# Performance work log

Hardware: AMD Instinct MI355X
Metric: run time of the kernel (lower is better)

## Reference

```python
import jax, jax.numpy as jnp
import numpy as np


def conv2d(x, w, b, pad):
    # NCHW / OIHW conv, stride 1
    y = jax.lax.conv_general_dilated(x, w, (1, 1), [(pad, pad), (pad, pad)],
                                     dimension_numbers=('NCHW', 'OIHW', 'NCHW'))
    return y + b[None, :, None, None]


def deform_conv2d(x, offset, modulator, w_reg, b_reg):
    # Faithful reimplementation of torchvision.ops.deform_conv2d (stride=1,
    # pad=K//2, dilation=1, 1 offset group), offset layout [B, 2*K*K, H, W]
    # with (dy, dx) pairs per kernel tap.
    B, C, H, W = x.shape
    K = w_reg.shape[-1]
    KK = K * K
    pad = K // 2
    off = offset.reshape(B, KK, 2, H, W)
    ks_y = (jnp.arange(KK) // K - pad).astype(x.dtype)
    ks_x = (jnp.arange(KK) % K - pad).astype(x.dtype)
    hh = jnp.arange(H, dtype=x.dtype)
    ww = jnp.arange(W, dtype=x.dtype)
    # sampling coords per (batch, kernel tap, out_y, out_x)
    py = hh[None, None, :, None] + ks_y[None, :, None, None] + off[:, :, 0]
    px = ww[None, None, None, :] + ks_x[None, :, None, None] + off[:, :, 1]
    y0 = jnp.floor(py)
    x0 = jnp.floor(px)
    ly = py - y0
    lx = px - x0
    y0i = y0.astype(jnp.int32)
    x0i = x0.astype(jnp.int32)
    x_flat = x.reshape(B, C, H * W)

    def gather(yi, xi, wgt):
        valid = (yi >= 0) & (yi < H) & (xi >= 0) & (xi < W)
        idx = (jnp.clip(yi, 0, H - 1) * W + jnp.clip(xi, 0, W - 1)).reshape(B, KK, H * W)
        v = jnp.take_along_axis(x_flat[:, :, None, :], idx[:, None], axis=3)  # [B,C,KK,HW]
        w = (wgt * valid.astype(x.dtype)).reshape(B, 1, KK, H * W)
        return v * w

    v = (gather(y0i, x0i, (1 - ly) * (1 - lx))
         + gather(y0i, x0i + 1, (1 - ly) * lx)
         + gather(y0i + 1, x0i, ly * (1 - lx))
         + gather(y0i + 1, x0i + 1, ly * lx))
    v = v * modulator.reshape(B, 1, KK, H * W)
    out = jnp.einsum('bckn,ock->bon', v, w_reg.reshape(w_reg.shape[0], C, KK))
    return out.reshape(B, -1, H, W) + b_reg[None, :, None, None]


def setup_inputs() -> dict:
    key = jax.random.key(0)
    ks = jax.random.split(key, 14)
    B, C, H, W = 8, 256, 64, 64
    K = 3
    Cr = C // 4  # SE ratio=4
    x = jax.random.normal(ks[0], (B, C, H, W), jnp.float32)
    # small offset-conv weights keep sampled offsets modest (torchvision inits these to 0)
    w_off = jax.random.normal(ks[1], (2 * K * K, C, K, K), jnp.float32) * 0.01
    b_off = jax.random.normal(ks[2], (2 * K * K,), jnp.float32) * 0.01
    w_mod = jax.random.normal(ks[3], (K * K, C, K, K), jnp.float32) * 0.01
    b_mod = jax.random.normal(ks[4], (K * K,), jnp.float32) * 0.01
    w_reg = jax.random.normal(ks[5], (C, C, K, K), jnp.float32) * (1.0 / np.sqrt(C * K * K))
    b_reg = jax.random.normal(ks[6], (C,), jnp.float32) * 0.01
    w_se1 = jax.random.normal(ks[7], (Cr, C), jnp.float32) * (1.0 / np.sqrt(C))
    b_se1 = jnp.zeros((Cr,), jnp.float32)
    w_se2 = jax.random.normal(ks[8], (C, Cr), jnp.float32) * (1.0 / np.sqrt(Cr))
    b_se2 = jnp.zeros((C,), jnp.float32)
    w_mask = jax.random.normal(ks[9], (C, C, 1, 1), jnp.float32) * (1.0 / np.sqrt(C))
    b_mask = jnp.zeros((C,), jnp.float32)
    return {"x": x, "w_off": w_off, "b_off": b_off, "w_mod": w_mod, "b_mod": b_mod,
            "w_reg": w_reg, "b_reg": b_reg, "w_se1": w_se1, "b_se1": b_se1,
            "w_se2": w_se2, "b_se2": b_se2, "w_mask": w_mask, "b_mask": b_mask}


def reference(x, w_off, b_off, w_mod, b_mod, w_reg, b_reg,
              w_se1, b_se1, w_se2, b_se2, w_mask, b_mask):
    # DeformableConv2d
    offset = conv2d(x, w_off, b_off, pad=1)
    modulator = 2.0 * jax.nn.sigmoid(conv2d(x, w_mod, b_mod, pad=1))
    f = deform_conv2d(x, offset, modulator, w_reg, b_reg)
    # SEBlock('avg', ch, ratio=4)
    s = jnp.mean(f, axis=(2, 3))                       # [B, C]
    s = jax.nn.relu(s @ w_se1.T + b_se1)               # [B, C/4]
    s = jax.nn.sigmoid(s @ w_se2.T + b_se2)            # [B, C]
    f = f * s[:, :, None, None]
    # mask = Hardsigmoid(Conv1x1(x))
    m = conv2d(x, w_mask, b_mask, pad=0)
    m = jnp.clip(m / 6.0 + 0.5, 0.0, 1.0)
    return f * m + x
```

## Files before the change

kernel.cpp:

```cpp
#include <hip/hip_runtime.h>
#include <math.h>

#define HWSZ 4096
#define C_ 256
#define B_ 8

#define M_WS      0
#define XB_WS     4194304
#define WT2_WS    8388608
#define SMEAN_WS  8753152
#define SSCALE_WS 8755200

typedef __attribute__((ext_vector_type(8))) short short8;
typedef __attribute__((ext_vector_type(4))) float f32x4;

__device__ __forceinline__ uint bfr(float a) {
  uint u = __float_as_uint(a);
  return (u + 0x7fffu + ((u >> 16) & 1u)) >> 16;
}
__device__ __forceinline__ uint pk2(float a, float b) { return bfr(a) | (bfr(b) << 16); }
__device__ __forceinline__ float bff(ushort u) { return __uint_as_float((uint)u << 16); }
__device__ __forceinline__ float lo16(uint u) { return __uint_as_float(u << 16); }
__device__ __forceinline__ float hi16(uint u) { return __uint_as_float(u & 0xffff0000u); }

__global__ __launch_bounds__(256) void k0_weights(
    const float* __restrict__ w_reg, const float* __restrict__ w_mask,
    const float* __restrict__ w_off, const float* __restrict__ w_mod,
    float* __restrict__ ws) {
  int i = blockIdx.x * 256 + threadIdx.x;
  const int nwt = 10 * 65536;
  const int total = nwt + 9 * 32 * 256;
  if (i >= total) {
    int z = i - total;
    if (z < 2048) ws[SMEAN_WS + z] = 0.f;
    return;
  }
  float v;
  if (i < 9 * 65536) {
    int kk = i >> 16, o = (i >> 8) & 255, c = i & 255;
    v = w_reg[(o * C_ + c) * 9 + kk];
  } else if (i < nwt) {
    v = w_mask[i - 9 * 65536];
  } else {
    int e = i - nwt;
    int s = e >> 13, r = e & 8191;
    int o2 = r >> 8, c = r & 255;
    if (o2 < 18)      v = w_off[(o2 * C_ + c) * 9 + s];
    else if (o2 < 27) v = w_mod[((o2 - 18) * C_ + c) * 9 + s];
    else              v = 0.f;
  }
  ((ushort*)(ws + WT2_WS))[i] = (ushort)bfr(v);
}

__global__ __launch_bounds__(256) void k0b_nhwc(const float* __restrict__ x,
                                                float* __restrict__ ws) {
  __shared__ float tile[64][65];
  int b = blockIdx.x >> 6, hw0 = (blockIdx.x & 63) << 6;
  int t = threadIdx.x;
  uint* xb = (uint*)(ws + XB_WS) + ((size_t)b << 19);
  int rr = t >> 6, cc = t & 63;
  int e = t & 7, hwp = t >> 3;
  for (int cg = 0; cg < 4; cg++) {
    __syncthreads();
    const float* xp = x + ((size_t)(b * 256 + cg * 64 + rr)) * HWSZ + hw0 + cc;
    #pragma unroll
    for (int r0 = 0; r0 < 64; r0 += 4)
      tile[r0 + rr][cc] = xp[(size_t)r0 * HWSZ];
    __syncthreads();
    #pragma unroll
    for (int h2 = 0; h2 < 2; h2++) {
      int hw_l = h2 * 32 + hwp;
      int c2 = e * 8;
      uint4 val;
      val.x = pk2(tile[c2][hw_l], tile[c2 + 1][hw_l]);
      val.y = pk2(tile[c2 + 2][hw_l], tile[c2 + 3][hw_l]);
      val.z = pk2(tile[c2 + 4][hw_l], tile[c2 + 5][hw_l]);
      val.w = pk2(tile[c2 + 6][hw_l], tile[c2 + 7][hw_l]);
      *(uint4*)&xb[(size_t)(hw0 + hw_l) * 128 + cg * 32 + e * 4] = val;
    }
  }
}

__global__ __launch_bounds__(512, 4) void k2_fused(
    const float* __restrict__ b_off, const float* __restrict__ b_mod,
    const float* __restrict__ b_reg, const float* __restrict__ b_mask,
    float* __restrict__ ws, float* __restrict__ out) {
  __shared__ uint  vbuf32[64 * 128];
  __shared__ float offmod[27 * 64];
  __shared__ int   midx[9 * 4 * 64];
  __shared__ float mwgt[9 * 4 * 64];

  int bl = ((blockIdx.x & 7) << 6) | (blockIdx.x >> 3);
  int b = bl >> 6, h = bl & 63;
  int t = threadIdx.x;
  int lane = t & 63, w = t >> 6;
  const int hwid = (w << 1) | (lane >> 5);
  const int cl = lane & 31;
  const ushort* xb2 = (const ushort*)(ws + XB_WS) + ((size_t)b << 20);
  const ushort* wt2 = (const ushort*)(ws + WT2_WS);
  const ushort* wom = wt2 + 10 * 65536;
  const int fr = lane & 15, fq = lane >> 4;

  f32x4 aom = (f32x4)0.f;
  const int m0 = w >> 2, nt0 = w & 3;
  for (int s = 0; s < 9; s++) {
    int row = h + s / 3 - 1;
    uint4 pv[4];
    #pragma unroll
    for (int p = 0; p < 4; p++) {
      int n = p * 16 + hwid;
      int col = n + s % 3 - 1;
      uint4 d = make_uint4(0, 0, 0, 0);
      if (((unsigned)row < 64u) && ((unsigned)col < 64u))
        d = *(const uint4*)(xb2 + ((size_t)(row * 64 + col)) * 256 + cl * 8);
      pv[p] = d;
    }
    __syncthreads();
    #pragma unroll
    for (int p = 0; p < 4; p++) {
      int n = p * 16 + hwid;
      vbuf32[n * 128 + (((uint)(cl * 4)) ^ ((uint)(n & 7) << 2)) + 0] = pv[p].x;
      *(uint4*)&vbuf32[n * 128 + (((uint)(cl * 4)) ^ ((uint)(n & 7) << 2))] = pv[p];
    }
    __syncthreads();
    const ushort* wp = wom + (size_t)s * 8192;
    for (int ks = 0; ks < 8; ks++) {
      short8 af = *(const short8*)(wp + (m0 * 16 + fr) * 256 + ks * 32 + fq * 8);
      int bn = nt0 * 16 + fr;
      uint idx = (uint)bn * 128u + (((uint)(ks * 16 + fq * 4)) ^ ((uint)(bn & 7) << 2));
      short8 bf = *(const short8*)&vbuf32[idx];
      aom = __builtin_amdgcn_mfma_f32_16x16x32_bf16(af, bf, aom, 0, 0, 0);
    }
  }
  __syncthreads();
  #pragma unroll
  for (int r = 0; r < 4; r++) {
    int o = m0 * 16 + fq * 4 + r;
    int nn = nt0 * 16 + fr;
    if (o < 18) {
      offmod[o * 64 + nn] = aom[r] + b_off[o];
    } else if (o < 27) {
      float v = aom[r] + b_mod[o - 18];
      offmod[o * 64 + nn] = 2.f / (1.f + expf(-v));
    }
  }
  __syncthreads();

  for (int e = t; e < 576; e += 512) {
    int kk = e >> 6, p = e & 63;
    float dy = offmod[(2 * kk) * 64 + p];
    float dx = offmod[(2 * kk + 1) * 64 + p];
    float md = offmod[(18 + kk) * 64 + p];
    float py = (float)(h + kk / 3 - 1) + dy;
    float px = (float)(p + kk % 3 - 1) + dx;
    float fy = floorf(py), fx = floorf(px);
    float ly = py - fy, lx = px - fx;
    int y0 = (int)fy, x0 = (int)fx;
    int y1 = y0 + 1, x1 = x0 + 1;
    float vy0 = ((unsigned)y0 < 64u) ? 1.f : 0.f;
    float vy1 = ((unsigned)y1 < 64u) ? 1.f : 0.f;
    float vx0 = ((unsigned)x0 < 64u) ? 1.f : 0.f;
    float vx1 = ((unsigned)x1 < 64u) ? 1.f : 0.f;
    int cy0 = min(max(y0, 0), 63), cy1 = min(max(y1, 0), 63);
    int cx0 = min(max(x0, 0), 63), cx1 = min(max(x1, 0), 63);
    int base = kk * 256 + p;
    midx[base]       = cy0 * 64 + cx0;
    midx[base + 64]  = cy0 * 64 + cx1;
    midx[base + 128] = cy1 * 64 + cx0;
    midx[base + 192] = cy1 * 64 + cx1;
    mwgt[base]       = (1.f - ly) * (1.f - lx) * md * vy0 * vx0;
    mwgt[base + 64]  = (1.f - ly) * lx * md * vy0 * vx1;
    mwgt[base + 128] = ly * (1.f - lx) * md * vy1 * vx0;
    mwgt[base + 192] = ly * lx * md * vy1 * vx1;
  }
  __syncthreads();

  f32x4 acc[2][4];
  #pragma unroll
  for (int mt = 0; mt < 2; mt++)
    #pragma unroll
    for (int nt = 0; nt < 4; nt++) acc[mt][nt] = (f32x4)0.f;
  const int o0 = w << 5;

  for (int kk = 0; kk < 9; kk++) {
    uint4 pv[4];
    #pragma unroll
    for (int p = 0; p < 4; p++) {
      int n = p * 16 + hwid;
      int base = kk * 256 + n;
      float a0 = 0.f, a1 = 0.f, a2 = 0.f, a3 = 0.f, a4 = 0.f, a5 = 0.f, a6 = 0.f, a7 = 0.f;
      #pragma unroll
      for (int cr = 0; cr < 4; cr++) {
        int gi = midx[base + cr * 64];
        float wv = mwgt[base + cr * 64];
        uint4 d = *(const uint4*)(xb2 + (size_t)gi * 256 + cl * 8);
        a0 = fmaf(wv, lo16(d.x), a0); a1 = fmaf(wv, hi16(d.x), a1);
        a2 = fmaf(wv, lo16(d.y), a2); a3 = fmaf(wv, hi16(d.y), a3);
        a4 = fmaf(wv, lo16(d.z), a4); a5 = fmaf(wv, hi16(d.z), a5);
        a6 = fmaf(wv, lo16(d.w), a6); a7 = fmaf(wv, hi16(d.w), a7);
      }
      pv[p] = make_uint4(pk2(a0, a1), pk2(a2, a3), pk2(a4, a5), pk2(a6, a7));
    }
    __syncthreads();
    #pragma unroll
    for (int p = 0; p < 4; p++) {
      int n = p * 16 + hwid;
      *(uint4*)&vbuf32[n * 128 + (((uint)(cl * 4)) ^ ((uint)(n & 7) << 2))] = pv[p];
    }
    __syncthreads();
    const ushort* wtap = wt2 + (size_t)kk * 65536;
    for (int ks = 0; ks < 8; ks++) {
      short8 af0 = *(const short8*)(wtap + (o0 + fr) * 256 + ks * 32 + fq * 8);
      short8 af1 = *(const short8*)(wtap + (o0 + 16 + fr) * 256 + ks * 32 + fq * 8);
      #pragma unroll
      for (int nt = 0; nt < 4; nt++) {
        int bn = nt * 16 + fr;
        uint idx = (uint)bn * 128u + (((uint)(ks * 16 + fq * 4)) ^ ((uint)(bn & 7) << 2));
        short8 bf = *(const short8*)&vbuf32[idx];
        acc[0][nt] = __builtin_amdgcn_mfma_f32_16x16x32_bf16(af0, bf, acc[0][nt], 0, 0, 0);
        acc[1][nt] = __builtin_amdgcn_mfma_f32_16x16x32_bf16(af1, bf, acc[1][nt], 0, 0, 0);
      }
    }
  }
  float* sme = ws + SMEAN_WS + b * 256;
  #pragma unroll
  for (int mt = 0; mt < 2; mt++)
    #pragma unroll
    for (int r = 0; r < 4; r++) {
      int o = o0 + mt * 16 + fq * 4 + r;
      float bo = b_reg[o];
      float* op = out + (size_t)(b * C_ + o) * HWSZ + h * 64;
      float so = 0.f;
      #pragma unroll
      for (int nt = 0; nt < 4; nt++) {
        float fv = acc[mt][nt][r] + bo;
        op[nt * 16 + fr] = fv;
        so += fv;
        acc[mt][nt][r] = 0.f;
      }
      so += __shfl_xor(so, 1);
      so += __shfl_xor(so, 2);
      so += __shfl_xor(so, 4);
      so += __shfl_xor(so, 8);
      if (fr == 0) atomicAdd(&sme[o], so);
    }

  {
    uint4 pv[4];
    #pragma unroll
    for (int p = 0; p < 4; p++) {
      int n = p * 16 + hwid;
      pv[p] = *(const uint4*)(xb2 + ((size_t)(h * 64 + n)) * 256 + cl * 8);
    }
    __syncthreads();
    #pragma unroll
    for (int p = 0; p < 4; p++) {
      int n = p * 16 + hwid;
      *(uint4*)&vbuf32[n * 128 + (((uint)(cl * 4)) ^ ((uint)(n & 7) << 2))] = pv[p];
    }
    __syncthreads();
  }
  {
    const ushort* wtap = wt2 + (size_t)9 * 65536;
    for (int ks = 0; ks < 8; ks++) {
      short8 af0 = *(const short8*)(wtap + (o0 + fr) * 256 + ks * 32 + fq * 8);
      short8 af1 = *(const short8*)(wtap + (o0 + 16 + fr) * 256 + ks * 32 + fq * 8);
      #pragma unroll
      for (int nt = 0; nt < 4; nt++) {
        int bn = nt * 16 + fr;
        uint idx = (uint)bn * 128u + (((uint)(ks * 16 + fq * 4)) ^ ((uint)(bn & 7) << 2));
        short8 bf = *(const short8*)&vbuf32[idx];
        acc[0][nt] = __builtin_amdgcn_mfma_f32_16x16x32_bf16(af0, bf, acc[0][nt], 0, 0, 0);
        acc[1][nt] = __builtin_amdgcn_mfma_f32_16x16x32_bf16(af1, bf, acc[1][nt], 0, 0, 0);
      }
    }
  }
  ushort* mws = (ushort*)(ws + M_WS);
  #pragma unroll
  for (int mt = 0; mt < 2; mt++)
    #pragma unroll
    for (int r = 0; r < 4; r++) {
      int o = o0 + mt * 16 + fq * 4 + r;
      float bm = b_mask[o];
      ushort* mp = mws + (size_t)(b * C_ + o) * HWSZ + h * 64;
      #pragma unroll
      for (int nt = 0; nt < 4; nt++) {
        float mv = fminf(fmaxf((acc[mt][nt][r] + bm) * (1.f / 6.f) + 0.5f, 0.f), 1.f);
        mp[nt * 16 + fr] = (ushort)bfr(mv);
      }
    }
}

__global__ __launch_bounds__(256) void k4_se(
    const float* __restrict__ w_se1, const float* __restrict__ b_se1,
    const float* __restrict__ w_se2, const float* __restrict__ b_se2,
    float* __restrict__ ws) {
  __shared__ float sm[2048];
  __shared__ float s1[512];
  int t = threadIdx.x;
  for (int e = t; e < 2048; e += 256) sm[e] = ws[SMEAN_WS + e] * (1.f / HWSZ);
  __syncthreads();
  for (int e = t; e < 512; e += 256) {
    int b = e >> 6, cr = e & 63;
    float a = b_se1[cr];
    for (int c = 0; c < 256; c++) a += sm[b * 256 + c] * w_se1[cr * 256 + c];
    s1[e] = fmaxf(a, 0.f);
  }
  __syncthreads();
  for (int e = t; e < 2048; e += 256) {
    int b = e >> 8, c = e & 255;
    float a = b_se2[c];
    for (int cr = 0; cr < 64; cr++) a += s1[b * 64 + cr] * w_se2[c * 64 + cr];
    ws[SSCALE_WS + e] = 1.f / (1.f + expf(-a));
  }
}

__global__ __launch_bounds__(256) void k5_final(const float* __restrict__ x,
                                                const float* __restrict__ ws,
                                                float* __restrict__ out) {
  const ushort* mws = (const ushort*)(ws + M_WS);
  int i4 = blockIdx.x * 256 + threadIdx.x;
  const int total = B_ * C_ * HWSZ / 4;
  for (; i4 < total; i4 += gridDim.x * 256) {
    int i = i4 * 4;
    int bc = i >> 12;
    float s = ws[SSCALE_WS + bc];
    float4 f = *(const float4*)&out[i];
    uint2 mu = *(const uint2*)&mws[i];
    float4 xv = *(const float4*)&x[i];
    float4 r;
    r.x = f.x * s * bff((ushort)(mu.x & 0xffffu)) + xv.x;
    r.y = f.y * s * bff((ushort)(mu.x >> 16)) + xv.y;
    r.z = f.z * s * bff((ushort)(mu.y & 0xffffu)) + xv.z;
    r.w = f.w * s * bff((ushort)(mu.y >> 16)) + xv.w;
    *(float4*)&out[i] = r;
  }
}

extern "C" void kernel_launch(void* const* d_in, const int* in_sizes, int n_in,
                              void* d_out, int out_size, void* d_ws, size_t ws_size,
                              hipStream_t stream) {
  const float* x      = (const float*)d_in[0];
  const float* w_off  = (const float*)d_in[1];
  const float* b_off  = (const float*)d_in[2];
  const float* w_mod  = (const float*)d_in[3];
  const float* b_mod  = (const float*)d_in[4];
  const float* w_reg  = (const float*)d_in[5];
  const float* b_reg  = (const float*)d_in[6];
  const float* w_se1  = (const float*)d_in[7];
  const float* b_se1  = (const float*)d_in[8];
  const float* w_se2  = (const float*)d_in[9];
  const float* b_se2  = (const float*)d_in[10];
  const float* w_mask = (const float*)d_in[11];
  const float* b_mask = (const float*)d_in[12];
  float* out = (float*)d_out;
  float* ws  = (float*)d_ws;

  k0_weights<<<dim3(2856), dim3(256), 0, stream>>>(w_reg, w_mask, w_off, w_mod, ws);
  k0b_nhwc<<<dim3(512), dim3(256), 0, stream>>>(x, ws);
  k2_fused<<<dim3(512), dim3(512), 0, stream>>>(b_off, b_mod, b_reg, b_mask, ws, out);
  k4_se<<<dim3(1), dim3(256), 0, stream>>>(w_se1, b_se1, w_se2, b_se2, ws);
  k5_final<<<dim3(2048), dim3(256), 0, stream>>>(x, ws, out);
}
```

Baseline: 207.3 us.

## Double-buffer LDS and overlap bilinear gathers with MFMA in fused deform kernel

Replaces the single LDS staging buffer with two ping-pong buffers. Global loads for the next tap (shifted rows for the offset conv, bilinear gathers for the deform conv, centre rows for the mask conv) are issued before the current tap's MFMAs and written to the other buffer afterwards, which cuts the syncs per step from two to one. Sampling indices and weights are now computed per thread in registers instead of being staged in shared-memory tables. The cost is more live registers (eight uint4 gather results plus weights), which could cause spills at launch_bounds(512,4), and the layout doubles the LDS buffer size.

```diff
diff --git a/kernel.cpp b/kernel.cpp
--- a/kernel.cpp
+++ b/kernel.cpp
@@ -85,10 +85,8 @@
     const float* __restrict__ b_off, const float* __restrict__ b_mod,
     const float* __restrict__ b_reg, const float* __restrict__ b_mask,
     float* __restrict__ ws, float* __restrict__ out) {
-  __shared__ uint  vbuf32[64 * 128];
+  __shared__ uint vb[2][64 * 128];
   __shared__ float offmod[27 * 64];
-  __shared__ int   midx[9 * 4 * 64];
-  __shared__ float mwgt[9 * 4 * 64];
 
   int bl = ((blockIdx.x & 7) << 6) | (blockIdx.x >> 3);
   int b = bl >> 6, h = bl & 63;
@@ -101,58 +99,31 @@
   const ushort* wom = wt2 + 10 * 65536;
   const int fr = lane & 15, fq = lane >> 4;
 
-  f32x4 aom = (f32x4)0.f;
-  const int m0 = w >> 2, nt0 = w & 3;
-  for (int s = 0; s < 9; s++) {
+  int nrow[4]; uint widx[4];
+  #pragma unroll
+  for (int p = 0; p < 4; p++) {
+    nrow[p] = p * 16 + hwid;
+    widx[p] = (uint)nrow[p] * 128u + (((uint)cl * 4u) ^ ((uint)(nrow[p] & 7) << 2));
+  }
+
+  auto loadShift = [&](int s, uint4* d) {
     int row = h + s / 3 - 1;
-    uint4 pv[4];
     #pragma unroll
     for (int p = 0; p < 4; p++) {
-      int n = p * 16 + hwid;
-      int col = n + s % 3 - 1;
-      uint4 d = make_uint4(0, 0, 0, 0);
+      int col = nrow[p] + s % 3 - 1;
+      uint4 v = make_uint4(0, 0, 0, 0);
       if (((unsigned)row < 64u) && ((unsigned)col < 64u))
-        d = *(const uint4*)(xb2 + ((size_t)(row * 64 + col)) * 256 + cl * 8);
-      pv[p] = d;
-    }
-    __syncthreads();
-    #pragma unroll
-    for (int p = 0; p < 4; p++) {
-      int n = p * 16 + hwid;
-      vbuf32[n * 128 + (((uint)(cl * 4)) ^ ((uint)(n & 7) << 2)) + 0] = pv[p].x;
-      *(uint4*)&vbuf32[n * 128 + (((uint)(cl * 4)) ^ ((uint)(n & 7) << 2))] = pv[p];
-    }
-    __syncthreads();
-    const ushort* wp = wom + (size_t)s * 8192;
-    for (int ks = 0; ks < 8; ks++) {
-      short8 af = *(const short8*)(wp + (m0 * 16 + fr) * 256 + ks * 32 + fq * 8);
-      int bn = nt0 * 16 + fr;
-      uint idx = (uint)bn * 128u + (((uint)(ks * 16 + fq * 4)) ^ ((uint)(bn & 7) << 2));
-      short8 bf = *(const short8*)&vbuf32[idx];
-      aom = __builtin_amdgcn_mfma_f32_16x16x32_bf16(af, bf, aom, 0, 0, 0);
-    }
-  }
-  __syncthreads();
-  #pragma unroll
-  for (int r = 0; r < 4; r++) {
-    int o = m0 * 16 + fq * 4 + r;
-    int nn = nt0 * 16 + fr;
-    if (o < 18) {
-      offmod[o * 64 + nn] = aom[r] + b_off[o];
-    } else if (o < 27) {
-      float v = aom[r] + b_mod[o - 18];
-      offmod[o * 64 + nn] = 2.f / (1.f + expf(-v));
-    }
-  }
-  __syncthreads();
-
-  for (int e = t; e < 576; e += 512) {
-    int kk = e >> 6, p = e & 63;
-    float dy = offmod[(2 * kk) * 64 + p];
-    float dx = offmod[(2 * kk + 1) * 64 + p];
-    float md = offmod[(18 + kk) * 64 + p];
+        v = *(const uint4*)(xb2 + ((size_t)(row * 64 + col)) * 256 + cl * 8);
+      d[p] = v;
+    }
+  };
+  auto makeRecs = [&](int kk, int p, float* wg, int* ix) {
+    int n = nrow[p];
+    float dy = offmod[(2 * kk) * 64 + n];
+    float dx = offmod[(2 * kk + 1) * 64 + n];
+    float md = offmod[(18 + kk) * 64 + n];
     float py = (float)(h + kk / 3 - 1) + dy;
-    float px = (float)(p + kk % 3 - 1) + dx;
+    float px = (float)(n + kk % 3 - 1) + dx;
     float fy = floorf(py), fx = floorf(px);
     float ly = py - fy, lx = px - fx;
     int y0 = (int)fy, x0 = (int)fx;
@@ -163,15 +134,60 @@
     float vx1 = ((unsigned)x1 < 64u) ? 1.f : 0.f;
     int cy0 = min(max(y0, 0), 63), cy1 = min(max(y1, 0), 63);
     int cx0 = min(max(x0, 0), 63), cx1 = min(max(x1, 0), 63);
-    int base = kk * 256 + p;
-    midx[base]       = cy0 * 64 + cx0;
-    midx[base + 64]  = cy0 * 64 + cx1;
-    midx[base + 128] = cy1 * 64 + cx0;
-    midx[base + 192] = cy1 * 64 + cx1;
-    mwgt[base]       = (1.f - ly) * (1.f - lx) * md * vy0 * vx0;
-    mwgt[base + 64]  = (1.f - ly) * lx * md * vy0 * vx1;
-    mwgt[base + 128] = ly * (1.f - lx) * md * vy1 * vx0;
-    mwgt[base + 192] = ly * lx * md * vy1 * vx1;
+    ix[0] = cy0 * 64 + cx0; wg[0] = (1.f - ly) * (1.f - lx) * md * vy0 * vx0;
+    ix[1] = cy0 * 64 + cx1; wg[1] = (1.f - ly) * lx * md * vy0 * vx1;
+    ix[2] = cy1 * 64 + cx0; wg[2] = ly * (1.f - lx) * md * vy1 * vx0;
+    ix[3] = cy1 * 64 + cx1; wg[3] = ly * lx * md * vy1 * vx1;
+  };
+  auto combine = [&](const uint4* d, const float* wg) -> uint4 {
+    float a0 = 0.f, a1 = 0.f, a2 = 0.f, a3 = 0.f, a4 = 0.f, a5 = 0.f, a6 = 0.f, a7 = 0.f;
+    #pragma unroll
+    for (int cr = 0; cr < 4; cr++) {
+      uint4 dd = d[cr]; float wv = wg[cr];
+      a0 = fmaf(wv, lo16(dd.x), a0); a1 = fmaf(wv, hi16(dd.x), a1);
+      a2 = fmaf(wv, lo16(dd.y), a2); a3 = fmaf(wv, hi16(dd.y), a3);
+      a4 = fmaf(wv, lo16(dd.z), a4); a5 = fmaf(wv, hi16(dd.z), a5);
+      a6 = fmaf(wv, lo16(dd.w), a6); a7 = fmaf(wv, hi16(dd.w), a7);
+    }
+    return make_uint4(pk2(a0, a1), pk2(a2, a3), pk2(a4, a5), pk2(a6, a7));
+  };
+
+  f32x4 aom = (f32x4)0.f;
+  const int m0 = w >> 2, nt0 = w & 3;
+  {
+    uint4 sd[4];
+    loadShift(0, sd);
+    #pragma unroll
+    for (int p = 0; p < 4; p++) *(uint4*)&vb[0][widx[p]] = sd[p];
+    __syncthreads();
+    for (int s = 0; s < 9; s++) {
+      if (s < 8) loadShift(s + 1, sd);
+      const uint cur = s & 1;
+      const ushort* wp = wom + (size_t)s * 8192;
+      for (int ks = 0; ks < 8; ks++) {
+        short8 af = *(const short8*)(wp + (m0 * 16 + fr) * 256 + ks * 32 + fq * 8);
+        int bn = nt0 * 16 + fr;
+        uint idx = (uint)bn * 128u + (((uint)(ks * 16 + fq * 4)) ^ ((uint)(bn & 7) << 2));
+        short8 bf = *(const short8*)&vb[cur][idx];
+        aom = __builtin_amdgcn_mfma_f32_16x16x32_bf16(af, bf, aom, 0, 0, 0);
+      }
+      if (s < 8) {
+        #pragma unroll
+        for (int p = 0; p < 4; p++) *(uint4*)&vb[(s & 1) ^ 1][widx[p]] = sd[p];
+      }
+      __syncthreads();
+    }
+  }
+  #pragma unroll
+  for (int r = 0; r < 4; r++) {
+    int o = m0 * 16 + fq * 4 + r;
+    int nn = nt0 * 16 + fr;
+    if (o < 18) {
+      offmod[o * 64 + nn] = aom[r] + b_off[o];
+    } else if (o < 27) {
+      float v = aom[r] + b_mod[o - 18];
+      offmod[o * 64 + nn] = 2.f / (1.f + expf(-v));
+    }
   }
   __syncthreads();
 
@@ -181,101 +197,122 @@
     #pragma unroll
     for (int nt = 0; nt < 4; nt++) acc[mt][nt] = (f32x4)0.f;
   const int o0 = w << 5;
-
-  for (int kk = 0; kk < 9; kk++) {
-    uint4 pv[4];
+  float* sme = ws + SMEAN_WS + b * 256;
+  ushort* mws = (ushort*)(ws + M_WS);
+
+  {
     #pragma unroll
     for (int p = 0; p < 4; p++) {
-      int n = p * 16 + hwid;
-      int base = kk * 256 + n;
-      float a0 = 0.f, a1 = 0.f, a2 = 0.f, a3 = 0.f, a4 = 0.f, a5 = 0.f, a6 = 0.f, a7 = 0.f;
-      #pragma unroll
-      for (int cr = 0; cr < 4; cr++) {
-        int gi = midx[base + cr * 64];
-        float wv = mwgt[base + cr * 64];
-        uint4 d = *(const uint4*)(xb2 + (size_t)gi * 256 + cl * 8);
-        a0 = fmaf(wv, lo16(d.x), a0); a1 = fmaf(wv, hi16(d.x), a1);
-        a2 = fmaf(wv, lo16(d.y), a2); a3 = fmaf(wv, hi16(d.y), a3);
-        a4 = fmaf(wv, lo16(d.z), a4); a5 = fmaf(wv, hi16(d.z), a5);
-        a6 = fmaf(wv, lo16(d.w), a6); a7 = fmaf(wv, hi16(d.w), a7);
-      }
-      pv[p] = make_uint4(pk2(a0, a1), pk2(a2, a3), pk2(a4, a5), pk2(a6, a7));
-    }
-    __syncthreads();
-    #pragma unroll
-    for (int p = 0; p < 4; p++) {
-      int n = p * 16 + hwid;
-      *(uint4*)&vbuf32[n * 128 + (((uint)(cl * 4)) ^ ((uint)(n & 7) << 2))] = pv[p];
-    }
-    __syncthreads();
+      float wg[4]; int ix[4];
+      makeRecs(0, p, wg, ix);
+      uint4 d[4];
+      #pragma unroll
+      for (int cr = 0; cr < 4; cr++)
+        d[cr] = *(const uint4*)(xb2 + (size_t)ix[cr] * 256 + cl * 8);
+      *(uint4*)&vb[0][widx[p]] = combine(d, wg);
+    }
+  }
+  __syncthreads();
+
+  for (int kk = 0; kk < 10; kk++) {
+    const uint cur = kk & 1, nxt = cur ^ 1;
     const ushort* wtap = wt2 + (size_t)kk * 65536;
-    for (int ks = 0; ks < 8; ks++) {
+    const int nk = kk + 1;
+    uint4 d[8];
+    float wg01[8];
+    if (nk < 9) {
+      #pragma unroll
+      for (int p = 0; p < 2; p++) {
+        float wg[4]; int ix[4];
+        makeRecs(nk, p, wg, ix);
+        #pragma unroll
+        for (int cr = 0; cr < 4; cr++) {
+          d[p * 4 + cr] = *(const uint4*)(xb2 + (size_t)ix[cr] * 256 + cl * 8);
+          wg01[p * 4 + cr] = wg[cr];
+        }
+      }
+    } else if (nk == 9) {
+      #pragma unroll
+      for (int p = 0; p < 2; p++)
+        d[p * 4] = *(const uint4*)(xb2 + ((size_t)(h * 64 + nrow[p])) * 256 + cl * 8);
+    }
+    for (int ks = 0; ks < 4; ks++) {
       short8 af0 = *(const short8*)(wtap + (o0 + fr) * 256 + ks * 32 + fq * 8);
       short8 af1 = *(const short8*)(wtap + (o0 + 16 + fr) * 256 + ks * 32 + fq * 8);
       #pragma unroll
       for (int nt = 0; nt < 4; nt++) {
         int bn = nt * 16 + fr;
         uint idx = (uint)bn * 128u + (((uint)(ks * 16 + fq * 4)) ^ ((uint)(bn & 7) << 2));
-        short8 bf = *(const short8*)&vbuf32[idx];
+        short8 bf = *(const short8*)&vb[cur][idx];
         acc[0][nt] = __builtin_amdgcn_mfma_f32_16x16x32_bf16(af0, bf, acc[0][nt], 0, 0, 0);
         acc[1][nt] = __builtin_amdgcn_mfma_f32_16x16x32_bf16(af1, bf, acc[1][nt], 0, 0, 0);
       }
     }
-  }
-  float* sme = ws + SMEAN_WS + b * 256;
-  #pragma unroll
-  for (int mt = 0; mt < 2; mt++)
-    #pragma unroll
-    for (int r = 0; r < 4; r++) {
-      int o = o0 + mt * 16 + fq * 4 + r;
-      float bo = b_reg[o];
-      float* op = out + (size_t)(b * C_ + o) * HWSZ + h * 64;
-      float so = 0.f;
-      #pragma unroll
-      for (int nt = 0; nt < 4; nt++) {
-        float fv = acc[mt][nt][r] + bo;
-        op[nt * 16 + fr] = fv;
-        so += fv;
-        acc[mt][nt][r] = 0.f;
-      }
-      so += __shfl_xor(so, 1);
-      so += __shfl_xor(so, 2);
-      so += __shfl_xor(so, 4);
-      so += __shfl_xor(so, 8);
-      if (fr == 0) atomicAdd(&sme[o], so);
-    }
-
-  {
-    uint4 pv[4];
-    #pragma unroll
-    for (int p = 0; p < 4; p++) {
-      int n = p * 16 + hwid;
-      pv[p] = *(const uint4*)(xb2 + ((size_t)(h * 64 + n)) * 256 + cl * 8);
-    }
-    __syncthreads();
-    #pragma unroll
-    for (int p = 0; p < 4; p++) {
-      int n = p * 16 + hwid;
-      *(uint4*)&vbuf32[n * 128 + (((uint)(cl * 4)) ^ ((uint)(n & 7) << 2))] = pv[p];
-    }
-    __syncthreads();
-  }
-  {
-    const ushort* wtap = wt2 + (size_t)9 * 65536;
-    for (int ks = 0; ks < 8; ks++) {
+    if (nk < 9) {
+      *(uint4*)&vb[nxt][widx[0]] = combine(&d[0], &wg01[0]);
+      *(uint4*)&vb[nxt][widx[1]] = combine(&d[4], &wg01[4]);
+      #pragma unroll
+      for (int p = 2; p < 4; p++) {
+        float wg[4]; int ix[4];
+        makeRecs(nk, p, wg, ix);
+        #pragma unroll
+        for (int cr = 0; cr < 4; cr++) {
+          d[(p - 2) * 4 + cr] = *(const uint4*)(xb2 + (size_t)ix[cr] * 256 + cl * 8);
+          wg01[(p - 2) * 4 + cr] = wg[cr];
+        }
+      }
+    } else if (nk == 9) {
+      *(uint4*)&vb[nxt][widx[0]] = d[0];
+      *(uint4*)&vb[nxt][widx[1]] = d[4];
+      #pragma unroll
+      for (int p = 2; p < 4; p++)
+        d[(p - 2) * 4] = *(const uint4*)(xb2 + ((size_t)(h * 64 + nrow[p])) * 256 + cl * 8);
+    }
+    for (int ks = 4; ks < 8; ks++) {
       short8 af0 = *(const short8*)(wtap + (o0 + fr) * 256 + ks * 32 + fq * 8);
       short8 af1 = *(const short8*)(wtap + (o0 + 16 + fr) * 256 + ks * 32 + fq * 8);
       #pragma unroll
       for (int nt = 0; nt < 4; nt++) {
         int bn = nt * 16 + fr;
         uint idx = (uint)bn * 128u + (((uint)(ks * 16 + fq * 4)) ^ ((uint)(bn & 7) << 2));
-        short8 bf = *(const short8*)&vbuf32[idx];
+        short8 bf = *(const short8*)&vb[cur][idx];
         acc[0][nt] = __builtin_amdgcn_mfma_f32_16x16x32_bf16(af0, bf, acc[0][nt], 0, 0, 0);
         acc[1][nt] = __builtin_amdgcn_mfma_f32_16x16x32_bf16(af1, bf, acc[1][nt], 0, 0, 0);
       }
     }
-  }
-  ushort* mws = (ushort*)(ws + M_WS);
+    if (nk < 9) {
+      *(uint4*)&vb[nxt][widx[2]] = combine(&d[0], &wg01[0]);
+      *(uint4*)&vb[nxt][widx[3]] = combine(&d[4], &wg01[4]);
+    } else if (nk == 9) {
+      *(uint4*)&vb[nxt][widx[2]] = d[0];
+      *(uint4*)&vb[nxt][widx[3]] = d[4];
+    }
+    if (kk == 8) {
+      #pragma unroll
+      for (int mt = 0; mt < 2; mt++)
+        #pragma unroll
+        for (int r = 0; r < 4; r++) {
+          int o = o0 + mt * 16 + fq * 4 + r;
+          float bo = b_reg[o];
+          float* op = out + (size_t)(b * C_ + o) * HWSZ + h * 64;
+          float so = 0.f;
+          #pragma unroll
+          for (int nt = 0; nt < 4; nt++) {
+            float fv = acc[mt][nt][r] + bo;
+            op[nt * 16 + fr] = fv;
+            so += fv;
+            acc[mt][nt][r] = 0.f;
+          }
+          so += __shfl_xor(so, 1);
+          so += __shfl_xor(so, 2);
+          so += __shfl_xor(so, 4);
+          so += __shfl_xor(so, 8);
+          if (fr == 0) atomicAdd(&sme[o], so);
+        }
+    }
+    if (kk < 9) __syncthreads();
+  }
+
   #pragma unroll
   for (int mt = 0; mt < 2; mt++)
     #pragma unroll
```

Result: slower. 228.3 us (+10.1%).
